# Kernel tuning notes

Hardware: AMD Instinct MI355X
Metric: run time of the kernel (lower is better)

The kernel has to match this reference:

```python
import jax, jax.numpy as jnp
import numpy as np

B, N, D, H = 16, 4096, 768, 16
E = D // H  # head dim = 48
EPS = 1e-12  # F.normalize eps


def setup_inputs() -> dict:
    key = jax.random.key(0)
    ks = jax.random.split(key, 10)
    s = 0.02
    return {
        "x": jax.random.normal(ks[0], (B, N, D), dtype=jnp.float32),
        "wq": jax.random.normal(ks[1], (D, D), dtype=jnp.float32) * s,
        "bq": jnp.zeros((D,), dtype=jnp.float32),
        "wk": jax.random.normal(ks[2], (D, D), dtype=jnp.float32) * s,
        "bk": jnp.zeros((D,), dtype=jnp.float32),
        "wv": jax.random.normal(ks[3], (D, D), dtype=jnp.float32) * s,
        "bv": jnp.zeros((D,), dtype=jnp.float32),
        "wo": jax.random.normal(ks[4], (D, D), dtype=jnp.float32) * s,
        "bo": jnp.zeros((D,), dtype=jnp.float32),
        "tau": jnp.float32(H),  # scalar learnable temperature, init = num_heads
    }


def _l2norm_seq(t):
    # F.normalize(t, p=2, dim=1): normalize over sequence axis n of [b, n, h, e]
    nrm = jnp.sqrt(jnp.sum(t * t, axis=1, keepdims=True))
    return t / jnp.maximum(nrm, EPS)


def reference(x, wq, bq, wk, bk, wv, bv, wo, bo, tau):
    b, n, d = x.shape
    q = (x @ wq.T + bq).reshape(b, n, H, E)
    k = (x @ wk.T + bk).reshape(b, n, H, E)
    v = (x @ wv.T + bv).reshape(b, n, H, E)
    q = _l2norm_seq(q)
    k = _l2norm_seq(k)
    # cross-covariance attention over feature dim: [b, e, h, q]
    energy = jnp.einsum('bnhe,bnhq->behq', q, k)
    attn = jax.nn.softmax(energy, axis=-1)
    out = jnp.einsum('behq,bnhe->bnhq', attn / tau, v)  # [b, n, h, e]
    out = out.reshape(b, n, d)
    return out @ wo.T + bo
```

## Files before the change

### kernel.cpp

```cpp
#include <hip/hip_runtime.h>
#include <hip/hip_bf16.h>

typedef __attribute__((ext_vector_type(8))) short bf16x8_t;
typedef __attribute__((ext_vector_type(4))) float f32x4_t;
typedef __attribute__((ext_vector_type(4))) float fv4;
typedef __attribute__((ext_vector_type(4))) unsigned short us4_t;
typedef __attribute__((ext_vector_type(8))) unsigned short us8_t;

static constexpr int BB = 16, NN = 4096, DD = 768, HH = 16, EE = 48;

__device__ __forceinline__ unsigned short f2bf(float f) {
  unsigned int u = __float_as_uint(f);
  u += 0x7fffu + ((u >> 16) & 1u);
  return (unsigned short)(u >> 16);
}
__device__ __forceinline__ float bf2f(unsigned short s) {
  unsigned int u = ((unsigned int)s) << 16;
  return __uint_as_float(u);
}

__device__ __forceinline__ void load_lds16(const void* g, void* l) {
  __builtin_amdgcn_global_load_lds((const __attribute__((address_space(1))) void*)g,
                                   (__attribute__((address_space(3))) void*)l, 16, 0, 0);
}

__device__ __forceinline__ void tcast64(const float* __restrict__ src, int sld,
                                        unsigned short* __restrict__ dst, int dld, int t)
{
  __shared__ float L[64][65];
#pragma unroll
  for (int q = 0; q < 4; ++q) {
    const int fi = t + q * 256;
    const int r = fi >> 4, c4 = fi & 15;
    fv4 v = *(const fv4*)(src + (long)r * sld + c4 * 4);
    L[r][c4 * 4 + 0] = v.x; L[r][c4 * 4 + 1] = v.y;
    L[r][c4 * 4 + 2] = v.z; L[r][c4 * 4 + 3] = v.w;
  }
  __syncthreads();
#pragma unroll
  for (int q = 0; q < 2; ++q) {
    const int wi = t + q * 256;
    const int rr = wi >> 3, ng = wi & 7;
    us8_t o;
#pragma unroll
    for (int j = 0; j < 8; ++j) o[j] = f2bf(L[ng * 8 + j][rr]);
    *(us8_t*)(dst + (long)rr * dld + ng * 8) = o;
  }
  __syncthreads();
}

__global__ __launch_bounds__(256) void transpose_cast_x(
    const float* __restrict__ x, unsigned short* __restrict__ xb,
    unsigned short* __restrict__ xbT, float* __restrict__ xsum)
{
  __shared__ float L[64][65];
  __shared__ float csum[64];
  const int nx = blockIdx.x, dx = blockIdx.y, b = blockIdx.z;
  const int n0 = nx * 64, d0 = dx * 64;
  const int t = threadIdx.x;
  if (t < 64) csum[t] = 0.f;
  const float* src = x + ((long)b * NN + n0) * DD + d0;
  unsigned short* thru = xb + ((long)b * NN + n0) * DD + d0;
  unsigned short* dst = xbT + ((long)b * DD + d0) * NN + n0;
#pragma unroll
  for (int q = 0; q < 4; ++q) {
    const int fi = t + q * 256;
    const int r = fi >> 4, c4 = fi & 15;
    fv4 v = *(const fv4*)(src + (long)r * DD + c4 * 4);
    L[r][c4 * 4 + 0] = v.x; L[r][c4 * 4 + 1] = v.y;
    L[r][c4 * 4 + 2] = v.z; L[r][c4 * 4 + 3] = v.w;
    us4_t o; o.x = f2bf(v.x); o.y = f2bf(v.y); o.z = f2bf(v.z); o.w = f2bf(v.w);
    *(us4_t*)(thru + (long)r * DD + c4 * 4) = o;
  }
  __syncthreads();
#pragma unroll
  for (int q = 0; q < 2; ++q) {
    const int wi = t + q * 256;
    const int rr = wi >> 3, ng = wi & 7;
    us8_t o; float s8 = 0.f;
#pragma unroll
    for (int j = 0; j < 8; ++j) { float v = L[ng * 8 + j][rr]; o[j] = f2bf(v); s8 += v; }
    *(us8_t*)(dst + (long)rr * NN + ng * 8) = o;
    atomicAdd(&csum[rr], s8);
  }
  __syncthreads();
  if (t < 64) atomicAdd(&xsum[(long)b * DD + d0 + t], csum[t]);
}

__global__ __launch_bounds__(256) void small_cast(
    const float* __restrict__ wq, const float* __restrict__ wk, const float* __restrict__ wv,
    unsigned short* __restrict__ W2, unsigned short* __restrict__ wvT,
    float* __restrict__ zeros, float* __restrict__ xsum)
{
  const int blk = blockIdx.x, t = threadIdx.x;
  if (blk < 576) {
#pragma unroll
    for (int q = 0; q < 2; ++q) {
      long g = (long)blk * 512 + t * 2 + q;
      long e0 = g * 4;
      int row = (int)(e0 / DD), col = (int)(e0 % DD);
      const float* src = (row < DD) ? (wq + (long)row * DD + col)
                                    : (wk + (long)(row - DD) * DD + col);
      fv4 v = *(const fv4*)src;
      us4_t o; o.x = f2bf(v.x); o.y = f2bf(v.y); o.z = f2bf(v.z); o.w = f2bf(v.w);
      *(us4_t*)(W2 + e0) = o;
    }
  } else if (blk < 720) {
    const int tile = blk - 576;
    const int ti = tile / 12, tj = tile % 12;
    const int k0 = ti * 64, i0 = tj * 64;
    tcast64(wv + (long)i0 * DD + k0, DD, wvT + (long)k0 * DD + i0, DD, t);
  } else if (blk == 720) {
#pragma unroll
    for (int q = 0; q < 4; ++q) zeros[t * 4 + q] = 0.f;
  } else {
#pragma unroll
    for (int q = 0; q < 4; ++q) xsum[(long)(blk - 721) * 1024 + t * 4 + q] = 0.f;
  }
}

template<int OUT_BF16, int SYM>
__global__ __launch_bounds__(256) void gemm_bt(
    const unsigned short* __restrict__ A, int lda, long aStride,
    const unsigned short* __restrict__ Bt, int ldb, long bStride,
    void* __restrict__ Cv, int ldc, long cStride,
    const float* __restrict__ bias, long biasStride, int K,
    int perB, int nt)
{
  __shared__ unsigned short As[128 * 64];
  __shared__ unsigned short Bs[128 * 64];
  const int nwg = gridDim.x;
  const int bid = blockIdx.x;
  const int wid = (bid & 7) * (nwg >> 3) + (bid >> 3);
  const int zb = wid / perB;
  const int t0 = wid % perB;
  int i0, j0;
  if (SYM) {
    int tt = t0; i0 = 0;
    while (tt >= nt - i0) { tt -= nt - i0; ++i0; }
    j0 = i0 + tt;
  } else {
    i0 = t0 / nt; j0 = t0 % nt;
  }
  const unsigned short* Ab = A + (long)zb * aStride;
  const unsigned short* Bb = Bt + (long)zb * bStride;
  const float* bz = bias + (long)zb * biasStride;
  const long m0 = (long)i0 * 128;
  const int n0 = j0 * 128;
  const int t = threadIdx.x;
  const int wave = t >> 6, lane = t & 63;
  const int wr = wave >> 1, wc = wave & 1;

  f32x4_t acc[4][4] = {};

  const int srow = t >> 3;
  const long scol = (long)(((t & 7) ^ (srow & 7)) << 3);
  unsigned short* ldsA = As + wave * 512;
  unsigned short* ldsB = Bs + wave * 512;

  for (int kt = 0; kt < K; kt += 64) {
#pragma unroll
    for (int p = 0; p < 4; ++p) {
      load_lds16(Ab + (m0 + p * 32 + srow) * (long)lda + kt + scol, ldsA + p * 2048);
      load_lds16(Bb + (long)(n0 + p * 32 + srow) * ldb + kt + scol, ldsB + p * 2048);
    }
    __syncthreads();
#pragma unroll
    for (int kk = 0; kk < 2; ++kk) {
      const int cswz = (((kk << 2) + (lane >> 4)) ^ (lane & 7)) << 4;
      bf16x8_t af[4], bfr[4];
#pragma unroll
      for (int f = 0; f < 4; ++f) {
        af[f]  = *(const bf16x8_t*)((const char*)As + (wr * 64 + f * 16 + (lane & 15)) * 128 + cswz);
        bfr[f] = *(const bf16x8_t*)((const char*)Bs + (wc * 64 + f * 16 + (lane & 15)) * 128 + cswz);
      }
#pragma unroll
      for (int i = 0; i < 4; ++i)
#pragma unroll
        for (int j = 0; j < 4; ++j)
          acc[i][j] = __builtin_amdgcn_mfma_f32_16x16x32_bf16(af[i], bfr[j], acc[i][j], 0, 0, 0);
    }
    __syncthreads();
  }

  const int col_l = lane & 15;
  const int rbase = (lane >> 4) << 2;
#pragma unroll
  for (int i = 0; i < 4; ++i) {
    const long growb = m0 + wr * 64 + i * 16 + rbase;
#pragma unroll
    for (int j = 0; j < 4; ++j) {
      const int col = n0 + wc * 64 + j * 16 + col_l;
      if (OUT_BF16) {
        const float bcol = bz[col];
        us4_t o;
#pragma unroll
        for (int r = 0; r < 4; ++r) o[r] = f2bf(acc[i][j][r] + bcol);
        unsigned short* cb = (unsigned short*)Cv + (long)zb * cStride;
#pragma unroll
        for (int r = 0; r < 4; ++r) cb[(growb + r) * ldc + col] = o[r];
        if (SYM && i0 != j0)
          *(us4_t*)(cb + (long)col * ldc + growb) = o;
      } else {
        float* cbase = (float*)Cv + (long)zb * cStride;
#pragma unroll
        for (int r = 0; r < 4; ++r)
          cbase[(growb + r) * ldc + col] = acc[i][j][r] + bz[col];
      }
    }
  }
}

#define GP_STRIDE 2464

__global__ __launch_bounds__(256) void energy_partial2(
    const unsigned short* __restrict__ T, const unsigned short* __restrict__ W2,
    float* __restrict__ Gp)
{
  __shared__ unsigned short Ts[2][48 * 128];
  __shared__ unsigned short Ws[2][48 * 128];
  __shared__ float G_sh[2448];

  const int kc = blockIdx.x, h = blockIdx.y, b = blockIdx.z;
  const int t = threadIdx.x;
  const int wave = t >> 6, lane = t & 63;

  for (int i = t; i < 2448; i += 256) G_sh[i] = 0.f;

  f32x4_t accG[3][3] = {};
  f32x4_t accQ[3] = {};
  f32x4_t accK[3] = {};

  long qoff[3];
#pragma unroll
  for (int p = 0; p < 3; ++p) {
    const int L = p * 4096 + wave * 1024 + lane * 16;
    const int e = L >> 8;
    const int blk = (L >> 4) & 15;
    const int sblk = blk ^ (e & 7);
    qoff[p] = (long)e * DD + sblk * 8;
  }
  const unsigned short* Tq = T + ((long)b * 1536 + h * 48) * DD;
  const unsigned short* Tk = Tq + (long)DD * DD;
  const unsigned short* Wq = W2 + (long)h * 48 * DD;
  const unsigned short* Wk = Wq + (long)DD * DD;

  int foff[3];
#pragma unroll
  for (int f = 0; f < 3; ++f) {
    const int e = f * 16 + (lane & 15);
    foff[f] = e * 256 + (((wave * 4 + (lane >> 4)) ^ (e & 7)) << 4);
  }
  __syncthreads();

  for (int ci = 0; ci < 3; ++ci) {
    const int col0 = kc * 384 + ci * 128;
#pragma unroll
    for (int p = 0; p < 3; ++p) {
      load_lds16(Tq + qoff[p] + col0, &Ts[0][p * 2048] + wave * 512);
      load_lds16(Tk + qoff[p] + col0, &Ts[1][p * 2048] + wave * 512);
      load_lds16(Wq + qoff[p] + col0, &Ws[0][p * 2048] + wave * 512);
      load_lds16(Wk + qoff[p] + col0, &Ws[1][p * 2048] + wave * 512);
    }
    __syncthreads();
    bf16x8_t tq[3], tk[3], wqf[3], wkf[3];
#pragma unroll
    for (int f = 0; f < 3; ++f) {
      tq[f]  = *(const bf16x8_t*)((const char*)&Ts[0][0] + foff[f]);
      tk[f]  = *(const bf16x8_t*)((const char*)&Ts[1][0] + foff[f]);
      wqf[f] = *(const bf16x8_t*)((const char*)&Ws[0][0] + foff[f]);
      wkf[f] = *(const bf16x8_t*)((const char*)&Ws[1][0] + foff[f]);
    }
#pragma unroll
    for (int i = 0; i < 3; ++i) {
      accQ[i] = __builtin_amdgcn_mfma_f32_16x16x32_bf16(tq[i], wqf[i], accQ[i], 0, 0, 0);
      accK[i] = __builtin_amdgcn_mfma_f32_16x16x32_bf16(tk[i], wkf[i], accK[i], 0, 0, 0);
#pragma unroll
      for (int j = 0; j < 3; ++j)
        accG[i][j] = __builtin_amdgcn_mfma_f32_16x16x32_bf16(tq[i], wkf[j], accG[i][j], 0, 0, 0);
    }
    __syncthreads();
  }

#pragma unroll
  for (int i = 0; i < 3; ++i)
#pragma unroll
    for (int j = 0; j < 3; ++j) {
      int e = i * 16 + ((lane >> 4) << 2);
      int qi = j * 16 + (lane & 15);
#pragma unroll
      for (int r = 0; r < 4; ++r) atomicAdd(&G_sh[(e + r) * 49 + qi], accG[i][j][r]);
    }
  if ((lane >> 4) == ((lane & 15) >> 2)) {
    int r = (lane & 15) & 3;
#pragma unroll
    for (int f = 0; f < 3; ++f) {
      atomicAdd(&G_sh[2352 + f * 16 + (lane & 15)], accQ[f][r]);
      atomicAdd(&G_sh[2400 + f * 16 + (lane & 15)], accK[f][r]);
    }
  }
  __syncthreads();

  float* out = Gp + (long)(((b * HH + h) << 1) + kc) * GP_STRIDE;
  for (int i = t; i < 2448; i += 256) out[i] = G_sh[i];
}

__global__ __launch_bounds__(256) void energy_finish2(
    const float* __restrict__ Gp, const float* __restrict__ xsum,
    const float* __restrict__ wq, const float* __restrict__ wk,
    const float* __restrict__ bq, const float* __restrict__ bk,
    const float* __restrict__ tau_p, unsigned short* __restrict__ A_out)
{
  __shared__ float G_sh[2448];
  __shared__ float vq[48], vk[48], bqs[48], bks[48];
  __shared__ int has_bias;
  const int h = blockIdx.x, b = blockIdx.y;
  const int t = threadIdx.x;

  const float* base = Gp + (long)((b * HH + h) << 1) * GP_STRIDE;
  for (int i = t; i < 2448; i += 256)
    G_sh[i] = base[i] + base[GP_STRIDE + i];
  if (t < 48) { bqs[t] = bq[h * 48 + t]; bks[t] = bk[h * 48 + t]; }
  __syncthreads();
  if (t == 0) {
    float s = 0.f;
    for (int i = 0; i < 48; ++i) s += fabsf(bqs[i]) + fabsf(bks[i]);
    has_bias = (s != 0.f);
  }
  __syncthreads();
  if (has_bias) {
    if (t < 96) {
      const int e = t < 48 ? t : t - 48;
      const float* wrow = (t < 48 ? wq : wk) + (long)(h * 48 + e) * DD;
      const float* xs = xsum + (long)b * DD;
      float s = 0.f;
      for (int g = 0; g < DD / 4; ++g) {
        fv4 a = *(const fv4*)(wrow + g * 4);
        fv4 c = *(const fv4*)(xs + g * 4);
        s += a.x * c.x + a.y * c.y + a.z * c.z + a.w * c.w;
      }
      if (t < 48) vq[e] = s; else vk[e] = s;
    }
  } else if (t < 48) { vq[t] = 0.f; vk[t] = 0.f; }
  __syncthreads();

  if (t < 48) {
    const float tau = *tau_p;
    const float nq2c = G_sh[2352 + t] + 2.f * bqs[t] * vq[t] + (float)NN * bqs[t] * bqs[t];
    const float nq = fmaxf(sqrtf(nq2c), 1e-12f);
    float row[48];
    float mx = -1e30f;
#pragma unroll 1
    for (int qi = 0; qi < 48; ++qi) {
      float nk2c = G_sh[2400 + qi] + 2.f * bks[qi] * vk[qi] + (float)NN * bks[qi] * bks[qi];
      float nk = fmaxf(sqrtf(nk2c), 1e-12f);
      float e = G_sh[t * 49 + qi] + vq[t] * bks[qi] + bqs[t] * vk[qi]
              + (float)NN * bqs[t] * bks[qi];
      float g = e / (nq * nk);
      row[qi] = g; mx = fmaxf(mx, g);
    }
    float s = 0.f;
#pragma unroll 1
    for (int qi = 0; qi < 48; ++qi) { row[qi] = __expf(row[qi] - mx); s += row[qi]; }
    const float inv = 1.f / (s * tau);
    unsigned short* dst = A_out + (((long)b * HH + h) * 48) * 64 + (long)t * 64;
#pragma unroll 1
    for (int qi = 0; qi < 48; ++qi) dst[qi] = f2bf(row[qi] * inv);
#pragma unroll 1
    for (int qi = 48; qi < 64; ++qi) dst[qi] = 0;
  }
}

__global__ __launch_bounds__(256) void build_btf(
    const unsigned short* __restrict__ A_ws, const float* __restrict__ wo,
    unsigned short* __restrict__ btf)
{
  __shared__ unsigned short Wsh[128 * 72];
  __shared__ unsigned short Ash[48 * 72];
  const int nchunk = blockIdx.x, h = blockIdx.y, b = blockIdx.z;
  const int t = threadIdx.x;
  const int wave = t >> 6, lane = t & 63;
  const int no0 = nchunk * 128;

  for (int i = t; i < 128 * 64; i += 256) {
    int r = i >> 6, c = i & 63;
    Wsh[r * 72 + c] = (c < 48) ? f2bf(wo[(long)(no0 + r) * DD + h * 48 + c]) : (unsigned short)0;
  }
  const unsigned short* Asrc = A_ws + ((long)b * HH + h) * 48 * 64;
  for (int i = t; i < 48 * 64; i += 256) {
    int r = i >> 6, c = i & 63;
    Ash[r * 72 + c] = Asrc[r * 64 + c];
  }
  __syncthreads();

  f32x4_t acc[2][3] = {};
#pragma unroll
  for (int ks = 0; ks < 2; ++ks) {
    const int k0 = ks * 32 + ((lane >> 4) << 3);
    bf16x8_t af[2], bfr[3];
#pragma unroll
    for (int mi = 0; mi < 2; ++mi)
      af[mi] = *(const bf16x8_t*)&Wsh[(wave * 32 + mi * 16 + (lane & 15)) * 72 + k0];
#pragma unroll
    for (int nj = 0; nj < 3; ++nj)
      bfr[nj] = *(const bf16x8_t*)&Ash[(nj * 16 + (lane & 15)) * 72 + k0];
#pragma unroll
    for (int mi = 0; mi < 2; ++mi)
#pragma unroll
      for (int nj = 0; nj < 3; ++nj)
        acc[mi][nj] = __builtin_amdgcn_mfma_f32_16x16x32_bf16(af[mi], bfr[nj], acc[mi][nj], 0, 0, 0);
  }

  const int col_l = lane & 15;
  const int rbase = (lane >> 4) << 2;
#pragma unroll
  for (int mi = 0; mi < 2; ++mi)
#pragma unroll
    for (int r = 0; r < 4; ++r) {
      int no = no0 + wave * 32 + mi * 16 + rbase + r;
      unsigned short* dst = btf + ((long)b * DD + no) * DD + h * 48;
#pragma unroll
      for (int nj = 0; nj < 3; ++nj)
        dst[nj * 16 + col_l] = f2bf(acc[mi][nj][r]);
    }
}

__global__ __launch_bounds__(256) void build_bias2(
    const unsigned short* __restrict__ btf, const float* __restrict__ bv,
    const float* __restrict__ bo, float* __restrict__ bias2)
{
  const int bx = blockIdx.x, b = blockIdx.y;
  const int wave = threadIdx.x >> 6, lane = threadIdx.x & 63;
  const int j = bx * 4 + wave;
  const unsigned short* row = btf + ((long)b * DD + j) * DD;
  float s = 0.f;
#pragma unroll
  for (int ii = 0; ii < 12; ++ii) {
    int i = ii * 64 + lane;
    s += bf2f(row[i]) * bv[i];
  }
#pragma unroll
  for (int off = 32; off > 0; off >>= 1) s += __shfl_down(s, off);
  if (lane == 0) bias2[(long)b * DD + j] = bo[j] + s;
}

extern "C" void kernel_launch(void* const* d_in, const int* in_sizes, int n_in,
                              void* d_out, int out_size, void* d_ws, size_t ws_size,
                              hipStream_t stream)
{
  (void)in_sizes; (void)n_in; (void)out_size;
  const float* x   = (const float*)d_in[0];
  const float* wq  = (const float*)d_in[1];
  const float* bq  = (const float*)d_in[2];
  const float* wk  = (const float*)d_in[3];
  const float* bk  = (const float*)d_in[4];
  const float* wv  = (const float*)d_in[5];
  const float* bv  = (const float*)d_in[6];
  const float* wo  = (const float*)d_in[7];
  const float* bo  = (const float*)d_in[8];
  const float* tau = (const float*)d_in[9];

  char* ws = (char*)d_ws;
  unsigned short* xb    = (unsigned short*)(ws + 0L);
  unsigned short* xbT   = (unsigned short*)(ws + 100663296L);
  unsigned short* S     = (unsigned short*)(ws + 201326592L);
  unsigned short* T     = (unsigned short*)(ws + 220200960L);
  unsigned short* W2    = (unsigned short*)(ws + 257949696L);
  unsigned short* wvT   = (unsigned short*)(ws + 260308992L);
  float*          zeros = (float*)         (ws + 261488640L);
  float*          xsum  = (float*)         (ws + 261492736L);
  float*          Gp    = (float*)         (ws + 261541888L);
  unsigned short* A_ws  = (unsigned short*)(ws + 266588160L);
  unsigned short* btf   = (unsigned short*)(ws + 268161024L);
  unsigned short* Ctf   = (unsigned short*)(ws + 287035392L);
  float*          bias2 = (float*)         (ws + 305909760L);
  if (ws_size < 305958912ULL) return;

  small_cast<<<733, 256, 0, stream>>>(wq, wk, wv, W2, wvT, zeros, xsum);
  transpose_cast_x<<<dim3(64, 12, BB), 256, 0, stream>>>(x, xb, xbT, xsum);

  gemm_bt<1, 1><<<16 * 21, 256, 0, stream>>>(
      xbT, NN, (long)DD * NN, xbT, NN, (long)DD * NN,
      S, DD, (long)DD * DD, zeros, 0L, NN, 21, 6);

  gemm_bt<1, 0><<<16 * 72, 256, 0, stream>>>(
      W2, DD, 0L, S, DD, (long)DD * DD,
      T, DD, (long)1536 * DD, zeros, 0L, DD, 72, 6);

  energy_partial2<<<dim3(2, HH, BB), 256, 0, stream>>>(T, W2, Gp);
  energy_finish2<<<dim3(HH, BB), 256, 0, stream>>>(Gp, xsum, wq, wk, bq, bk, tau, A_ws);

  build_btf<<<dim3(6, HH, BB), 256, 0, stream>>>(A_ws, wo, btf);
  build_bias2<<<dim3(192, BB), 256, 0, stream>>>(btf, bv, bo, bias2);

  gemm_bt<1, 0><<<16 * 36, 256, 0, stream>>>(
      btf, DD, (long)DD * DD, wvT, DD, 0L,
      Ctf, DD, (long)DD * DD, zeros, 0L, DD, 36, 6);

  gemm_bt<0, 0><<<16 * 192, 256, 0, stream>>>(
      xb, DD, (long)NN * DD, Ctf, DD, (long)DD * DD,
      d_out, DD, (long)NN * DD, bias2, (long)DD, DD, 192, 6);
}
```

Before: 505.6 us.

## Use 256x256-tile 512-thread GEMM with XCD-aware block remap for final projection

Replaces the final batched output GEMM (x times folded per-batch weight plus bias) with a new kernel using 256x256 output tiles, 8 waves per block, double-buffered direct-to-LDS loads with an XOR swizzle, and a block-index remap that spreads consecutive tiles across XCDs. Larger tiles raise arithmetic intensity and cut redundant global/L2 traffic for this dominant GEMM. In exchange it uses 128 KB of LDS and a large accumulator array per thread, which limits occupancy and adds register pressure, and the grid drops to 768 blocks.

```diff
diff --git a/kernel.cpp b/kernel.cpp
--- a/kernel.cpp
+++ b/kernel.cpp
@@ -207,6 +207,104 @@
         for (int r = 0; r < 4; ++r)
           cbase[(growb + r) * ldc + col] = acc[i][j][r] + bz[col];
       }
+    }
+  }
+}
+
+__global__ __launch_bounds__(512, 2) void gemm256(
+    const unsigned short* __restrict__ A, int lda, long aStride,
+    const unsigned short* __restrict__ Bt, int ldb, long bStride,
+    float* __restrict__ C, int ldc, long cStride,
+    const float* __restrict__ bias, long biasStride, int K,
+    int perB, int nt)
+{
+  __shared__ unsigned short As[2 * 256 * 64];
+  __shared__ unsigned short Bs[2 * 256 * 64];
+  char* AsB = (char*)As;
+  char* BsB = (char*)Bs;
+
+  const int nwg = gridDim.x;
+  const int bid = blockIdx.x;
+  const int wid = (bid & 7) * (nwg >> 3) + (bid >> 3);
+  const int zb = wid / perB;
+  const int t0 = wid % perB;
+  const int i0 = t0 / nt, j0 = t0 % nt;
+  const unsigned short* Ab = A + (long)zb * aStride;
+  const unsigned short* Bb = Bt + (long)zb * bStride;
+  const float* bz = bias + (long)zb * biasStride;
+  const long m0 = (long)i0 * 256;
+  const int n0 = j0 * 256;
+  const int t = threadIdx.x;
+  const int wave = t >> 6, lane = t & 63;
+  const int wr = wave >> 2, wc = wave & 3;
+
+  f32x4_t acc[8][4] = {};
+
+  const int srow = t >> 3;
+  const long scol = (long)(((t & 7) ^ ((t >> 3) & 7)) << 3);
+  const int nkt = K >> 6;
+
+  auto STAGE = [&](int bsel, int kt) {
+    const long kc = (long)kt * 64 + scol;
+#pragma unroll
+    for (int p = 0; p < 4; ++p) {
+      load_lds16(Ab + (m0 + p * 64 + srow) * (long)lda + kc,
+                 AsB + bsel * 32768 + p * 8192 + wave * 1024);
+      load_lds16(Bb + (long)(n0 + p * 64 + srow) * ldb + kc,
+                 BsB + bsel * 32768 + p * 8192 + wave * 1024);
+    }
+  };
+
+  STAGE(0, 0);
+  if (nkt > 1) STAGE(1, 1);
+
+  const int lan15 = lane & 15, lan7 = lane & 7, kgrp = lane >> 4;
+
+  for (int kt = 0; kt < nkt; ++kt) {
+    if (kt + 1 < nkt) { asm volatile("s_waitcnt vmcnt(8)" ::: "memory"); }
+    else              { asm volatile("s_waitcnt vmcnt(0)" ::: "memory"); }
+    __builtin_amdgcn_sched_barrier(0);
+    __builtin_amdgcn_s_barrier();
+    __builtin_amdgcn_sched_barrier(0);
+    const int bsel = kt & 1;
+#pragma unroll
+    for (int kk = 0; kk < 2; ++kk) {
+      const int cswz = (((kk << 2) + kgrp) ^ lan7) << 4;
+      bf16x8_t af[8], bfr[4];
+#pragma unroll
+      for (int mf = 0; mf < 8; ++mf)
+        af[mf] = *(const bf16x8_t*)(AsB + bsel * 32768 + wr * 16384
+                                    + (mf * 16 + lan15) * 128 + cswz);
+#pragma unroll
+      for (int nf = 0; nf < 4; ++nf) {
+        const int rb = wc * 64 + nf * 16 + lan15;
+        bfr[nf] = *(const bf16x8_t*)(BsB + bsel * 32768 + (rb >> 7) * 16384
+                                     + (rb & 127) * 128 + cswz);
+      }
+#pragma unroll
+      for (int mf = 0; mf < 8; ++mf)
+#pragma unroll
+        for (int nf = 0; nf < 4; ++nf)
+          acc[mf][nf] = __builtin_amdgcn_mfma_f32_16x16x32_bf16(af[mf], bfr[nf], acc[mf][nf], 0, 0, 0);
+    }
+    __builtin_amdgcn_sched_barrier(0);
+    __builtin_amdgcn_s_barrier();
+    __builtin_amdgcn_sched_barrier(0);
+    if (kt + 2 < nkt) STAGE(bsel, kt + 2);
+  }
+
+  const int rbase = (lane >> 4) << 2;
+  float* Cb = C + (long)zb * cStride;
+#pragma unroll
+  for (int mf = 0; mf < 8; ++mf) {
+    const long growb = m0 + wr * 128 + mf * 16 + rbase;
+#pragma unroll
+    for (int nf = 0; nf < 4; ++nf) {
+      const int col = n0 + wc * 64 + nf * 16 + lan15;
+      const float bcol = bz[col];
+#pragma unroll
+      for (int r = 0; r < 4; ++r)
+        Cb[(growb + r) * ldc + col] = acc[mf][nf][r] + bcol;
     }
   }
 }
@@ -497,7 +595,7 @@
       btf, DD, (long)DD * DD, wvT, DD, 0L,
       Ctf, DD, (long)DD * DD, zeros, 0L, DD, 36, 6);
 
-  gemm_bt<0, 0><<<16 * 192, 256, 0, stream>>>(
+  gemm256<<<768, 512, 0, stream>>>(
       xb, DD, (long)NN * DD, Ctf, DD, (long)DD * DD,
-      d_out, DD, (long)NN * DD, bias2, (long)DD, DD, 192, 6);
-}
+      (float*)d_out, DD, (long)NN * DD, bias2, (long)DD, DD, 48, 3);
+}
```

New measurement: 502.9 us, median of 2. About the same (-0.5%).
